# Optimization experiments

Hardware: AMD Instinct MI355X
Metric: run time of the kernel (lower is better)

## Reference

```python
import jax, jax.numpy as jnp
import numpy as np

D = 1024
HEADS = 16
HEAD_DIM = D // HEADS
EPS = 1e-5


def layer_norm(x, gamma, beta):
    mu = jnp.mean(x, axis=-1, keepdims=True)
    var = jnp.mean(jnp.square(x - mu), axis=-1, keepdims=True)
    return (x - mu) * jax.lax.rsqrt(var + EPS) * gamma + beta


def setup_inputs() -> dict:
    key = jax.random.key(0)
    ks = jax.random.split(key, 8)
    B, S = 4, 2048
    s_in = 1.0 / np.sqrt(D)
    s_ffn = 1.0 / np.sqrt(4 * D)
    return {
        "x": jax.random.normal(ks[0], (B, S, D), dtype=jnp.float32),
        "ln1_g": jnp.ones((D,), jnp.float32),
        "ln1_b": jnp.zeros((D,), jnp.float32),
        "w_qkv": jax.random.uniform(ks[1], (D, 3 * D), jnp.float32, -s_in, s_in),
        "b_qkv": jnp.zeros((3 * D,), jnp.float32),
        "w_out": jax.random.uniform(ks[2], (D, D), jnp.float32, -s_in, s_in),
        "b_out": jnp.zeros((D,), jnp.float32),
        "ln2_g": jnp.ones((D,), jnp.float32),
        "ln2_b": jnp.zeros((D,), jnp.float32),
        "w_ffn1": jax.random.uniform(ks[3], (D, 4 * D), jnp.float32, -s_in, s_in),
        "b_ffn1": jnp.zeros((4 * D,), jnp.float32),
        "w_ffn2": jax.random.uniform(ks[4], (4 * D, D), jnp.float32, -s_ffn, s_ffn),
        "b_ffn2": jnp.zeros((D,), jnp.float32),
    }


def reference(x, ln1_g, ln1_b, w_qkv, b_qkv, w_out, b_out,
              ln2_g, ln2_b, w_ffn1, b_ffn1, w_ffn2, b_ffn2):
    B, S, Dm = x.shape
    h = layer_norm(x, ln1_g, ln1_b)
    qkv = h @ w_qkv + b_qkv  # [B,S,3D]
    q, k, v = jnp.split(qkv, 3, axis=-1)
    # [B,S,D] -> [B,H,S,hd]
    def to_heads(t):
        return t.reshape(B, S, HEADS, HEAD_DIM).transpose(0, 2, 1, 3)
    q, k, v = to_heads(q), to_heads(k), to_heads(v)
    scores = jnp.einsum('bhqd,bhkd->bhqk', q, k) / np.sqrt(HEAD_DIM).astype(np.float32)
    attn = jax.nn.softmax(scores, axis=-1)
    out = jnp.einsum('bhqk,bhkd->bhqd', attn, v)
    out = out.transpose(0, 2, 1, 3).reshape(B, S, Dm)
    x = x + (out @ w_out + b_out)
    h = layer_norm(x, ln2_g, ln2_b)
    h = jax.nn.gelu(h @ w_ffn1 + b_ffn1, approximate=False) @ w_ffn2 + b_ffn2
    return x + h
```

## Files before the change

kernel.cpp:

```cpp
#include <hip/hip_runtime.h>
#include <cstdint>
#include <cstddef>

typedef unsigned short u16;
typedef unsigned int   u32;
typedef __bf16 bf16x8 __attribute__((ext_vector_type(8)));
typedef float  f32x4  __attribute__((ext_vector_type(4)));
static_assert(sizeof(bf16x8) == 16, "bf16x8 must be 16B");
static_assert(sizeof(f32x4) == 16, "f32x4 must be 16B");

#define DEVI static __device__ __forceinline__

#define QSCALE 0.18033688011112042f

DEVI u16 f2bf(float x) {
  u32 u = __builtin_bit_cast(u32, x);
  u = (u + 0x7FFFu + ((u >> 16) & 1u)) >> 16;
  return (u16)u;
}

DEVI void gload16(const u16* g, u16* l) {
  __builtin_amdgcn_global_load_lds(
      (const __attribute__((address_space(1))) void*)g,
      (__attribute__((address_space(3))) void*)l, 16, 0, 0);
}

#define S_BARRIER() asm volatile("s_barrier" ::: "memory")
#define VMCNT(n) asm volatile("s_waitcnt vmcnt(" #n ")" ::: "memory")

template <int MO, int NACC>
DEVI void mm16(f32x4 (&acc)[NACC][4], const bf16x8 (&af)[4], const bf16x8 (&bf)[4]) {
  __builtin_amdgcn_s_setprio(1);
#pragma unroll
  for (int m = 0; m < 4; m++)
#pragma unroll
    for (int n = 0; n < 4; n++)
      acc[MO + m][n] =
          __builtin_amdgcn_mfma_f32_16x16x32_bf16(af[m], bf[n], acc[MO + m][n], 0, 0, 0);
  __builtin_amdgcn_s_setprio(0);
}

__global__ __launch_bounds__(256) void transpose_cvt(const float* __restrict__ W,
                                                     u16* __restrict__ WT,
                                                     int K, int N,
                                                     float scale, int nscale) {
  __shared__ float tile[32][33];
  int tx = threadIdx.x & 31, ty = threadIdx.x >> 5;
  int c0 = blockIdx.x * 32, r0 = blockIdx.y * 32;
#pragma unroll
  for (int i = 0; i < 4; i++)
    tile[ty + i * 8][tx] = W[(size_t)(r0 + ty + i * 8) * N + c0 + tx];
  __syncthreads();
#pragma unroll
  for (int i = 0; i < 4; i++) {
    int r = ty + i * 8;
    int n = c0 + r;
    float scl = (n < nscale) ? scale : 1.f;
    WT[(size_t)n * K + r0 + tx] = f2bf(tile[tx][r] * scl);
  }
}

__global__ __launch_bounds__(256) void prep_bias(const float* __restrict__ b,
                                                 float* __restrict__ o) {
  int i = blockIdx.x * 256 + threadIdx.x;
  o[i] = b[i] * (i < 1024 ? QSCALE : 1.f);
}

__global__ __launch_bounds__(256) void ln_k(const float* __restrict__ X,
                                            const float* __restrict__ gam,
                                            const float* __restrict__ bet,
                                            u16* __restrict__ H) {
  __shared__ float2 part[4];
  int row = blockIdx.x, t = threadIdx.x;
  const float4* xr = (const float4*)(X + (size_t)row * 1024);
  float4 v = xr[t];
  float s = v.x + v.y + v.z + v.w;
  float q = v.x * v.x + v.y * v.y + v.z * v.z + v.w * v.w;
#pragma unroll
  for (int o = 32; o > 0; o >>= 1) {
    s += __shfl_xor(s, o);
    q += __shfl_xor(q, o);
  }
  if ((t & 63) == 0) part[t >> 6] = make_float2(s, q);
  __syncthreads();
  float S = part[0].x + part[1].x + part[2].x + part[3].x;
  float Q = part[0].y + part[1].y + part[2].y + part[3].y;
  float mu = S * (1.f / 1024.f);
  float rs = rsqrtf(Q * (1.f / 1024.f) - mu * mu + 1e-5f);
  float4 gv = ((const float4*)gam)[t];
  float4 bv = ((const float4*)bet)[t];
  ushort4 o;
  o.x = f2bf((v.x - mu) * rs * gv.x + bv.x);
  o.y = f2bf((v.y - mu) * rs * gv.y + bv.y);
  o.z = f2bf((v.z - mu) * rs * gv.z + bv.z);
  o.w = f2bf((v.w - mu) * rs * gv.w + bv.w);
  *(ushort4*)(H + (size_t)row * 1024 + t * 4) = o;
}

template <int EPI, int NACC>
DEVI void epilogue(f32x4 (&acc)[NACC][4], const float* bias, const float* res,
                   float* outF, u16* outB, int N, int rbase, int cbase, int g, int li) {
#pragma unroll
  for (int n = 0; n < 4; n++) {
    int c = cbase + n * 16 + li;
    float bv = bias[c];
#pragma unroll
    for (int a = 0; a < NACC; a++) {
      int rowb = rbase + a * 16 + g * 4;
#pragma unroll
      for (int r = 0; r < 4; r++) {
        size_t idx = (size_t)(rowb + r) * N + c;
        float v = acc[a][n][r] + bv;
        if constexpr (EPI == 1) {
          v += res[idx];
          outF[idx] = v;
        } else if constexpr (EPI == 2) {
          v = 0.5f * v * (1.f + erff(v * 0.70710678118654752f));
          outB[idx] = f2bf(v);
        } else {
          outB[idx] = f2bf(v);
        }
      }
    }
  }
}

template <int EPI>
__global__ __launch_bounds__(1024, 4) void gemm256(const u16* __restrict__ A,
                                                   const u16* __restrict__ Bt,
                                                   const float* __restrict__ bias,
                                                   const float* __restrict__ res,
                                                   float* __restrict__ outF,
                                                   u16* __restrict__ outB,
                                                   int M, int N, int K) {
  __shared__ uint4 As[2][2048];
  __shared__ uint4 Bs[2][2048];
  const int t = threadIdx.x, lane = t & 63, wv = t >> 6;
  const int wr = wv >> 2, wc = wv & 3;
  const int li = lane & 15, g = lane >> 4;

  const int gx = gridDim.x;
  const int nwg = gx * gridDim.y;
  const int wg = blockIdx.y * gx + blockIdx.x;
  const int swz = (wg & 7) * (nwg >> 3) + (wg >> 3);
  const int bx = swz % gx, by = swz / gx;
  const int bm0 = by * 256, bn0 = bx * 256;

  f32x4 acc[4][4];
  const f32x4 z4 = {0.f, 0.f, 0.f, 0.f};
#pragma unroll
  for (int a = 0; a < 4; a++)
#pragma unroll
    for (int n = 0; n < 4; n++) acc[a][n] = z4;

  const u16* aB = A + (size_t)(bm0 + wv * 16 + li) * K + g * 8;
  const u16* bB = Bt + (size_t)(bn0 + wv * 16 + li) * K + g * 8;

  auto stA = [&](int buf, int kh, int kt) {
    gload16(aB + (size_t)kt * 64 + kh * 32, (u16*)&As[buf][(kh * 16 + wv) * 64]);
  };
  auto stB = [&](int buf, int kh, int kt) {
    gload16(bB + (size_t)kt * 64 + kh * 32, (u16*)&Bs[buf][(kh * 16 + wv) * 64]);
  };

  stA(0, 0, 0); stB(0, 0, 0);
  stA(0, 1, 0); stB(0, 1, 0);
  VMCNT(2);
  S_BARRIER();

  const int NT = K >> 6;
  int cur = 0;
  for (int kt = 0; kt < NT; kt++) {
    const int nx = cur ^ 1;
    const bool more = (kt + 1 < NT);
    bf16x8 af[4], bf[4];
#pragma unroll
    for (int n = 0; n < 4; n++)
      bf[n] = __builtin_bit_cast(bf16x8, Bs[cur][(wc * 4 + n) * 64 + lane]);
#pragma unroll
    for (int m = 0; m < 4; m++)
      af[m] = __builtin_bit_cast(bf16x8, As[cur][(wr * 4 + m) * 64 + lane]);
    if (more) { stA(nx, 0, kt + 1); stB(nx, 0, kt + 1); }
    S_BARRIER();
    mm16<0>(acc, af, bf);
    if (more) { VMCNT(2); } else { VMCNT(0); }
    S_BARRIER();
#pragma unroll
    for (int n = 0; n < 4; n++)
      bf[n] = __builtin_bit_cast(bf16x8, Bs[cur][(16 + wc * 4 + n) * 64 + lane]);
#pragma unroll
    for (int m = 0; m < 4; m++)
      af[m] = __builtin_bit_cast(bf16x8, As[cur][(16 + wr * 4 + m) * 64 + lane]);
    if (more) { stA(nx, 1, kt + 1); stB(nx, 1, kt + 1); }
    S_BARRIER();
    mm16<0>(acc, af, bf);
    if (more) { VMCNT(2); }
    S_BARRIER();
    cur = nx;
  }

  epilogue<EPI>(acc, bias, res, outF, outB, N, bm0 + wr * 64, bn0 + wc * 64, g, li);
}

template <int EPI>
__global__ __launch_bounds__(512, 1) void gemm128(const u16* __restrict__ A,
                                                  const u16* __restrict__ Bt,
                                                  const float* __restrict__ bias,
                                                  const float* __restrict__ res,
                                                  float* __restrict__ outF,
                                                  u16* __restrict__ outB,
                                                  int M, int N, int K) {
  __shared__ uint4 As[2][1024];
  __shared__ uint4 Bs[2][2048];
  const int t = threadIdx.x, lane = t & 63, wv = t >> 6;
  const int wr = wv >> 2, wc = wv & 3;
  const int li = lane & 15, g = lane >> 4;

  const int gx = gridDim.x;
  const int nwg = gx * gridDim.y;
  const int wg = blockIdx.y * gx + blockIdx.x;
  const int swz = (wg & 7) * (nwg >> 3) + (wg >> 3);
  const int bx = swz % gx, by = swz / gx;
  const int bm0 = by * 128, bn0 = bx * 256;

  f32x4 acc[4][4];
  const f32x4 z4 = {0.f, 0.f, 0.f, 0.f};
#pragma unroll
  for (int a = 0; a < 4; a++)
#pragma unroll
    for (int n = 0; n < 4; n++) acc[a][n] = z4;

  const u16* aB = A + (size_t)(bm0 + wv * 16 + li) * K + g * 8;
  const u16* bB = Bt + (size_t)(bn0 + wv * 16 + li) * K + g * 8;
  const size_t rskip = (size_t)128 * K;

  auto stA = [&](int buf, int j, int kt) {
    gload16(aB + (size_t)kt * 64 + j * 32, (u16*)&As[buf][(j * 8 + wv) * 64]);
  };
  auto stB = [&](int buf, int j, int kt) {
    gload16(bB + (size_t)kt * 64 + ((j & 1) ? rskip : (size_t)0) + (j >> 1) * 32,
            (u16*)&Bs[buf][(j * 8 + wv) * 64]);
  };

  stA(0, 0, 0); stB(0, 0, 0); stB(0, 1, 0);
  stA(0, 1, 0); stB(0, 2, 0); stB(0, 3, 0);
  VMCNT(3);
  S_BARRIER();

  const int NT = K >> 6;
  int cur = 0;
  for (int kt = 0; kt < NT; kt++) {
    const int nx = cur ^ 1;
    const bool more = (kt + 1 < NT);
    bf16x8 af[4], bf[4];
#pragma unroll
    for (int n = 0; n < 4; n++)
      bf[n] = __builtin_bit_cast(bf16x8, Bs[cur][(wc * 4 + n) * 64 + lane]);
#pragma unroll
    for (int m = 0; m < 4; m++)
      af[m] = __builtin_bit_cast(bf16x8, As[cur][(wr * 4 + m) * 64 + lane]);
    if (more) { stA(nx, 0, kt + 1); stB(nx, 0, kt + 1); stB(nx, 1, kt + 1); }
    S_BARRIER();
    mm16<0>(acc, af, bf);
    if (more) { VMCNT(3); } else { VMCNT(0); }
    S_BARRIER();
#pragma unroll
    for (int n = 0; n < 4; n++)
      bf[n] = __builtin_bit_cast(bf16x8, Bs[cur][(16 + wc * 4 + n) * 64 + lane]);
#pragma unroll
    for (int m = 0; m < 4; m++)
      af[m] = __builtin_bit_cast(bf16x8, As[cur][(8 + wr * 4 + m) * 64 + lane]);
    if (more) { stA(nx, 1, kt + 1); stB(nx, 2, kt + 1); stB(nx, 3, kt + 1); }
    S_BARRIER();
    mm16<0>(acc, af, bf);
    if (more) { VMCNT(3); }
    S_BARRIER();
    cur = nx;
  }

  epilogue<EPI>(acc, bias, res, outF, outB, N, bm0 + wr * 64, bn0 + wc * 64, g, li);
}

__global__ __launch_bounds__(256) void v_tr(const u16* __restrict__ qkv,
                                            u16* __restrict__ vfm) {
  __shared__ u16 Vl[64 * 72];
  const int t = threadIdx.x;
  const int bh = blockIdx.y;
  const int bb = bh >> 4, h = bh & 15;
  const int kt = blockIdx.x;
#pragma unroll
  for (int bq = 0; bq < 2; bq++) {
    int c = t + bq * 256;
    int key = c >> 3, d0 = (c & 7) * 8;
    uint4 v = *(const uint4*)(qkv + (size_t)(bb * 2048 + kt * 64 + key) * 3072 + 2048 +
                              h * 64 + d0);
    *(uint4*)&Vl[key * 72 + d0] = v;
  }
  __syncthreads();
#pragma unroll
  for (int bq = 0; bq < 2; bq++) {
    int oc = t + bq * 256;
    int f = oc >> 6, l = oc & 63;
    int db = f >> 1, g32 = f & 1;
    int li = l & 15, g = l >> 4;
    u16 tmp[8];
#pragma unroll
    for (int e = 0; e < 8; e++) {
      int pk = g32 * 32 + ((e & 4) << 2) + g * 4 + (e & 3);
      tmp[e] = Vl[pk * 72 + db * 16 + li];
    }
    *(uint4*)(vfm + ((((size_t)bh * 32 + kt) * 8 + f) * 64 + l) * 8) = *(uint4*)tmp;
  }
}

__global__ __launch_bounds__(256) void attn_k(const u16* __restrict__ qkv,
                                              const u16* __restrict__ vfm,
                                              u16* __restrict__ ao) {
  __shared__ uint4 Ks[512];
  __shared__ uint4 Vs[512];
  const int t = threadIdx.x, lane = t & 63, wv = t >> 6;
  const int g = lane >> 4, li = lane & 15;
  const int bb = blockIdx.y >> 4, h = blockIdx.y & 15;
  const int q0 = blockIdx.x * 64 + wv * 16;

  const size_t qoff = (size_t)(bb * 2048 + q0 + li) * 3072 + h * 64 + g * 8;
  bf16x8 qf0 = __builtin_bit_cast(bf16x8, *(const uint4*)(qkv + qoff));
  bf16x8 qf1 = __builtin_bit_cast(bf16x8, *(const uint4*)(qkv + qoff + 32));

  const u16* kbase = qkv + (size_t)bb * 2048 * 3072 + 1024 + h * 64;
  const int f1 = wv + 4;
  const u16* ksrc0 = kbase + (size_t)(((wv >> 1) << 4) + li) * 3072 + ((wv & 1) << 5) + g * 8;
  const u16* ksrc1 = kbase + (size_t)(((f1 >> 1) << 4) + li) * 3072 + ((f1 & 1) << 5) + g * 8;
  const u16* vsrc0 = vfm + ((size_t)(bb * 16 + h) * 32) * 4096 + (wv * 64 + lane) * 8;
  const u16* vsrc1 = vsrc0 + 4 * 64 * 8;

  const f32x4 z4 = {0.f, 0.f, 0.f, 0.f};
  f32x4 Of[4];
#pragma unroll
  for (int db = 0; db < 4; db++) Of[db] = z4;
  f32x4 Ol = z4;

  bf16x8 vone;
#pragma unroll
  for (int j = 0; j < 8; j++) vone[j] = (__bf16)1.0f;

  for (int tile = 0; tile < 32; tile++) {
    __syncthreads();
    gload16(ksrc0 + (size_t)tile * 64 * 3072, (u16*)&Ks[wv * 64]);
    gload16(ksrc1 + (size_t)tile * 64 * 3072, (u16*)&Ks[(wv + 4) * 64]);
    gload16(vsrc0 + (size_t)tile * 4096, (u16*)&Vs[wv * 64]);
    gload16(vsrc1 + (size_t)tile * 4096, (u16*)&Vs[(wv + 4) * 64]);
    __syncthreads();

#pragma unroll
    for (int g32 = 0; g32 < 2; g32++) {
      bf16x8 pf;
#pragma unroll
      for (int tt = 0; tt < 2; tt++) {
        int kb16 = g32 * 2 + tt;
        bf16x8 k0f = __builtin_bit_cast(bf16x8, Ks[(kb16 * 2 + 0) * 64 + lane]);
        bf16x8 k1f = __builtin_bit_cast(bf16x8, Ks[(kb16 * 2 + 1) * 64 + lane]);
        f32x4 st = z4;
        st = __builtin_amdgcn_mfma_f32_16x16x32_bf16(k0f, qf0, st, 0, 0, 0);
        st = __builtin_amdgcn_mfma_f32_16x16x32_bf16(k1f, qf1, st, 0, 0, 0);
#pragma unroll
        for (int r = 0; r < 4; r++) pf[tt * 4 + r] = (__bf16)exp2f(st[r]);
      }
      __builtin_amdgcn_s_setprio(1);
#pragma unroll
      for (int db = 0; db < 4; db++) {
        bf16x8 vf = __builtin_bit_cast(bf16x8, Vs[(db * 2 + g32) * 64 + lane]);
        Of[db] = __builtin_amdgcn_mfma_f32_16x16x32_bf16(pf, vf, Of[db], 0, 0, 0);
      }
      Ol = __builtin_amdgcn_mfma_f32_16x16x32_bf16(pf, vone, Ol, 0, 0, 0);
      __builtin_amdgcn_s_setprio(0);
    }
  }

  float invl[4];
#pragma unroll
  for (int r = 0; r < 4; r++) invl[r] = 1.f / Ol[r];
#pragma unroll
  for (int db = 0; db < 4; db++)
#pragma unroll
    for (int r = 0; r < 4; r++)
      ao[(size_t)(bb * 2048 + q0 + 4 * g + r) * 1024 + h * 64 + db * 16 + li] =
          f2bf(Of[db][r] * invl[r]);
}

extern "C" void kernel_launch(void* const* d_in, const int* in_sizes, int n_in,
                              void* d_out, int out_size, void* d_ws, size_t ws_size,
                              hipStream_t stream) {
  const float* x = (const float*)d_in[0];
  const float* ln1g = (const float*)d_in[1];
  const float* ln1b = (const float*)d_in[2];
  const float* wqkv = (const float*)d_in[3];
  const float* bqkv = (const float*)d_in[4];
  const float* wout = (const float*)d_in[5];
  const float* bout = (const float*)d_in[6];
  const float* ln2g = (const float*)d_in[7];
  const float* ln2b = (const float*)d_in[8];
  const float* wff1 = (const float*)d_in[9];
  const float* bff1 = (const float*)d_in[10];
  const float* wff2 = (const float*)d_in[11];
  const float* bff2 = (const float*)d_in[12];
  float* outF = (float*)d_out;
  char* ws = (char*)d_ws;

  u16* wqkvT = (u16*)(ws + 0);
  u16* woutT = (u16*)(ws + 6291456);
  u16* wff1T = (u16*)(ws + 8388608);
  u16* wff2T = (u16*)(ws + 16777216);
  u16* hbuf  = (u16*)(ws + 25165824);
  u16* vfm   = (u16*)(ws + 25165824);
  u16* qkvb  = (u16*)(ws + 41943040);
  u16* attnb = (u16*)(ws + 92274688);
  u16* ffn1b = qkvb;
  float* biasq = (float*)attnb;

  transpose_cvt<<<dim3(96, 32), 256, 0, stream>>>(wqkv, wqkvT, 1024, 3072, QSCALE, 1024);
  transpose_cvt<<<dim3(32, 32), 256, 0, stream>>>(wout, woutT, 1024, 1024, 1.f, 0);
  transpose_cvt<<<dim3(128, 32), 256, 0, stream>>>(wff1, wff1T, 1024, 4096, 1.f, 0);
  transpose_cvt<<<dim3(32, 128), 256, 0, stream>>>(wff2, wff2T, 4096, 1024, 1.f, 0);
  prep_bias<<<12, 256, 0, stream>>>(bqkv, biasq);

  ln_k<<<8192, 256, 0, stream>>>(x, ln1g, ln1b, hbuf);
  gemm128<0><<<dim3(12, 64), 512, 0, stream>>>(hbuf, wqkvT, biasq, nullptr, nullptr, qkvb,
                                               8192, 3072, 1024);
  v_tr<<<dim3(32, 64), 256, 0, stream>>>(qkvb, vfm);
  attn_k<<<dim3(32, 64), 256, 0, stream>>>(qkvb, vfm, attnb);
  gemm128<1><<<dim3(4, 64), 512, 0, stream>>>(attnb, woutT, bout, x, outF, nullptr,
                                              8192, 1024, 1024);
  ln_k<<<8192, 256, 0, stream>>>(outF, ln2g, ln2b, hbuf);
  gemm256<2><<<dim3(16, 32), 1024, 0, stream>>>(hbuf, wff1T, bff1, nullptr, nullptr, ffn1b,
                                                8192, 4096, 1024);
  gemm128<1><<<dim3(4, 64), 512, 0, stream>>>(ffn1b, wff2T, bff2, outF, outF, nullptr,
                                              8192, 1024, 4096);

  (void)in_sizes;
  (void)n_in;
  (void)out_size;
  (void)ws_size;
}
```

Baseline: 477.0 us.

## Use 16-wave 128x256 GEMM with deeper prefetch and faster exp2/bf16 pack

Rewrites the 128x256 GEMM to run 16 waves per block, each owning a 32x64 sub-tile, with halved accumulators and a launch bound allowing several blocks per CU. The K loop now prefetches two tiles ahead with fewer barriers, and MFMA sections get raised priority. This is meant to improve latency hiding and occupancy. In attention, the softmax exponent uses the hardware exp2 builtin and packed bf16 conversion, which removes conversion overhead at some rounding/accuracy risk.

```diff
diff --git a/kernel.cpp b/kernel.cpp
--- a/kernel.cpp
+++ b/kernel.cpp
@@ -12,6 +12,12 @@
 #define DEVI static __device__ __forceinline__
 
 #define QSCALE 0.18033688011112042f
+
+#if __has_builtin(__builtin_amdgcn_exp2f)
+#define EXP2(x) __builtin_amdgcn_exp2f(x)
+#else
+#define EXP2(x) exp2f(x)
+#endif
 
 DEVI u16 f2bf(float x) {
   u32 u = __builtin_bit_cast(u32, x);
@@ -203,13 +209,13 @@
 }
 
 template <int EPI>
-__global__ __launch_bounds__(512, 1) void gemm128(const u16* __restrict__ A,
-                                                  const u16* __restrict__ Bt,
-                                                  const float* __restrict__ bias,
-                                                  const float* __restrict__ res,
-                                                  float* __restrict__ outF,
-                                                  u16* __restrict__ outB,
-                                                  int M, int N, int K) {
+__global__ __launch_bounds__(1024, 4) void gemm128w(const u16* __restrict__ A,
+                                                    const u16* __restrict__ Bt,
+                                                    const float* __restrict__ bias,
+                                                    const float* __restrict__ res,
+                                                    float* __restrict__ outF,
+                                                    u16* __restrict__ outB,
+                                                    int M, int N, int K) {
   __shared__ uint4 As[2][1024];
   __shared__ uint4 Bs[2][2048];
   const int t = threadIdx.x, lane = t & 63, wv = t >> 6;
@@ -223,62 +229,71 @@
   const int bx = swz % gx, by = swz / gx;
   const int bm0 = by * 128, bn0 = bx * 256;
 
-  f32x4 acc[4][4];
+  f32x4 acc[2][4];
   const f32x4 z4 = {0.f, 0.f, 0.f, 0.f};
 #pragma unroll
-  for (int a = 0; a < 4; a++)
+  for (int a = 0; a < 2; a++)
 #pragma unroll
     for (int n = 0; n < 4; n++) acc[a][n] = z4;
 
-  const u16* aB = A + (size_t)(bm0 + wv * 16 + li) * K + g * 8;
-  const u16* bB = Bt + (size_t)(bn0 + wv * 16 + li) * K + g * 8;
-  const size_t rskip = (size_t)128 * K;
-
-  auto stA = [&](int buf, int j, int kt) {
-    gload16(aB + (size_t)kt * 64 + j * 32, (u16*)&As[buf][(j * 8 + wv) * 64]);
+  const u16* aS = A + (size_t)(bm0 + (wv & 7) * 16 + li) * K + ((wv >> 3) << 5) + g * 8;
+  const u16* bS = Bt + (size_t)(bn0 + wv * 16 + li) * K + g * 8;
+
+  auto stage = [&](int buf, int kt) {
+    gload16(aS + (size_t)kt * 64, (u16*)&As[buf][wv * 64]);
+    gload16(bS + (size_t)kt * 64, (u16*)&Bs[buf][wv * 64]);
+    gload16(bS + (size_t)kt * 64 + 32, (u16*)&Bs[buf][(16 + wv) * 64]);
   };
-  auto stB = [&](int buf, int j, int kt) {
-    gload16(bB + (size_t)kt * 64 + ((j & 1) ? rskip : (size_t)0) + (j >> 1) * 32,
-            (u16*)&Bs[buf][(j * 8 + wv) * 64]);
-  };
-
-  stA(0, 0, 0); stB(0, 0, 0); stB(0, 1, 0);
-  stA(0, 1, 0); stB(0, 2, 0); stB(0, 3, 0);
+
+  stage(0, 0);
+  stage(1, 1);
   VMCNT(3);
   S_BARRIER();
 
   const int NT = K >> 6;
   int cur = 0;
   for (int kt = 0; kt < NT; kt++) {
-    const int nx = cur ^ 1;
-    const bool more = (kt + 1 < NT);
-    bf16x8 af[4], bf[4];
+    bf16x8 af[2], bf[4];
 #pragma unroll
     for (int n = 0; n < 4; n++)
       bf[n] = __builtin_bit_cast(bf16x8, Bs[cur][(wc * 4 + n) * 64 + lane]);
 #pragma unroll
-    for (int m = 0; m < 4; m++)
-      af[m] = __builtin_bit_cast(bf16x8, As[cur][(wr * 4 + m) * 64 + lane]);
-    if (more) { stA(nx, 0, kt + 1); stB(nx, 0, kt + 1); stB(nx, 1, kt + 1); }
-    S_BARRIER();
-    mm16<0>(acc, af, bf);
-    if (more) { VMCNT(3); } else { VMCNT(0); }
-    S_BARRIER();
+    for (int m = 0; m < 2; m++)
+      af[m] = __builtin_bit_cast(bf16x8, As[cur][(wr * 2 + m) * 64 + lane]);
+    __builtin_amdgcn_s_setprio(1);
+#pragma unroll
+    for (int m = 0; m < 2; m++)
+#pragma unroll
+      for (int n = 0; n < 4; n++)
+        acc[m][n] = __builtin_amdgcn_mfma_f32_16x16x32_bf16(af[m], bf[n], acc[m][n], 0, 0, 0);
+    __builtin_amdgcn_s_setprio(0);
 #pragma unroll
     for (int n = 0; n < 4; n++)
       bf[n] = __builtin_bit_cast(bf16x8, Bs[cur][(16 + wc * 4 + n) * 64 + lane]);
 #pragma unroll
-    for (int m = 0; m < 4; m++)
-      af[m] = __builtin_bit_cast(bf16x8, As[cur][(8 + wr * 4 + m) * 64 + lane]);
-    if (more) { stA(nx, 1, kt + 1); stB(nx, 2, kt + 1); stB(nx, 3, kt + 1); }
+    for (int m = 0; m < 2; m++)
+      af[m] = __builtin_bit_cast(bf16x8, As[cur][(8 + wr * 2 + m) * 64 + lane]);
+    __builtin_amdgcn_s_setprio(1);
+#pragma unroll
+    for (int m = 0; m < 2; m++)
+#pragma unroll
+      for (int n = 0; n < 4; n++)
+        acc[m][n] = __builtin_amdgcn_mfma_f32_16x16x32_bf16(af[m], bf[n], acc[m][n], 0, 0, 0);
+    __builtin_amdgcn_s_setprio(0);
+
     S_BARRIER();
-    mm16<0>(acc, af, bf);
-    if (more) { VMCNT(3); }
-    S_BARRIER();
-    cur = nx;
-  }
-
-  epilogue<EPI>(acc, bias, res, outF, outB, N, bm0 + wr * 64, bn0 + wc * 64, g, li);
+    if (kt + 2 < NT) {
+      stage(cur, kt + 2);
+      VMCNT(3);
+      S_BARRIER();
+    } else if (kt + 1 < NT) {
+      VMCNT(0);
+      S_BARRIER();
+    }
+    cur ^= 1;
+  }
+
+  epilogue<EPI>(acc, bias, res, outF, outB, N, bm0 + wr * 32, bn0 + wc * 64, g, li);
 }
 
 __global__ __launch_bounds__(256) void v_tr(const u16* __restrict__ qkv,
@@ -354,7 +369,7 @@
 
 #pragma unroll
     for (int g32 = 0; g32 < 2; g32++) {
-      bf16x8 pf;
+      uint4 pw;
 #pragma unroll
       for (int tt = 0; tt < 2; tt++) {
         int kb16 = g32 * 2 + tt;
@@ -363,9 +378,15 @@
         f32x4 st = z4;
         st = __builtin_amdgcn_mfma_f32_16x16x32_bf16(k0f, qf0, st, 0, 0, 0);
         st = __builtin_amdgcn_mfma_f32_16x16x32_bf16(k1f, qf1, st, 0, 0, 0);
-#pragma unroll
-        for (int r = 0; r < 4; r++) pf[tt * 4 + r] = (__bf16)exp2f(st[r]);
+        float e0 = EXP2(st[0]), e1 = EXP2(st[1]);
+        float e2 = EXP2(st[2]), e3 = EXP2(st[3]);
+        u32 wa, wb;
+        asm("v_cvt_pk_bf16_f32 %0, %1, %2" : "=v"(wa) : "v"(e0), "v"(e1));
+        asm("v_cvt_pk_bf16_f32 %0, %1, %2" : "=v"(wb) : "v"(e2), "v"(e3));
+        if (tt == 0) { pw.x = wa; pw.y = wb; }
+        else         { pw.z = wa; pw.w = wb; }
       }
+      bf16x8 pf = __builtin_bit_cast(bf16x8, pw);
       __builtin_amdgcn_s_setprio(1);
 #pragma unroll
       for (int db = 0; db < 4; db++) {
@@ -425,17 +446,17 @@
   prep_bias<<<12, 256, 0, stream>>>(bqkv, biasq);
 
   ln_k<<<8192, 256, 0, stream>>>(x, ln1g, ln1b, hbuf);
-  gemm128<0><<<dim3(12, 64), 512, 0, stream>>>(hbuf, wqkvT, biasq, nullptr, nullptr, qkvb,
-                                               8192, 3072, 1024);
+  gemm128w<0><<<dim3(12, 64), 1024, 0, stream>>>(hbuf, wqkvT, biasq, nullptr, nullptr, qkvb,
+                                                 8192, 3072, 1024);
   v_tr<<<dim3(32, 64), 256, 0, stream>>>(qkvb, vfm);
   attn_k<<<dim3(32, 64), 256, 0, stream>>>(qkvb, vfm, attnb);
-  gemm128<1><<<dim3(4, 64), 512, 0, stream>>>(attnb, woutT, bout, x, outF, nullptr,
-                                              8192, 1024, 1024);
+  gemm128w<1><<<dim3(4, 64), 1024, 0, stream>>>(attnb, woutT, bout, x, outF, nullptr,
+                                                8192, 1024, 1024);
   ln_k<<<8192, 256, 0, stream>>>(outF, ln2g, ln2b, hbuf);
   gemm256<2><<<dim3(16, 32), 1024, 0, stream>>>(hbuf, wff1T, bff1, nullptr, nullptr, ffn1b,
                                                 8192, 4096, 1024);
-  gemm128<1><<<dim3(4, 64), 512, 0, stream>>>(ffn1b, wff2T, bff2, outF, outF, nullptr,
-                                              8192, 1024, 4096);
+  gemm128w<1><<<dim3(4, 64), 1024, 0, stream>>>(ffn1b, wff2T, bff2, outF, outF, nullptr,
+                                                8192, 1024, 4096);
 
   (void)in_sizes;
   (void)n_in;
```

Measured after the change: 515.2 us. +8.0%, slower.
